# Performance work log

Measured on AMD Instinct MI355X. Metric: run time of the kernel, lower is better.

Reference implementation:

```python
import jax, jax.numpy as jnp
import numpy as np

T, B, IN, H = 256, 64, 512, 1024

def setup_inputs() -> dict:
    key = jax.random.key(0)
    ks = jax.random.split(key, 8)
    s_in = 1.0 / np.sqrt(IN)
    s_h = 1.0 / np.sqrt(H)
    return {
        "inp": jax.random.normal(ks[0], (T, B, IN), jnp.float32),
        "img": jax.random.normal(ks[1], (B, H), jnp.float32),
        "Wxh": jax.random.uniform(ks[2], (4 * H, IN), jnp.float32, -s_in, s_in),
        "bxh": jax.random.uniform(ks[3], (4 * H,), jnp.float32, -s_in, s_in),
        "Whh": jax.random.uniform(ks[4], (4 * H, H), jnp.float32, -s_h, s_h),
        "bhh": jax.random.uniform(ks[5], (4 * H,), jnp.float32, -s_h, s_h),
        "Wout": jax.random.uniform(ks[6], (IN, H), jnp.float32, -s_h, s_h),
        "bout": jax.random.uniform(ks[7], (IN,), jnp.float32, -s_h, s_h),
    }

def reference(inp, img, Wxh, bxh, Whh, bhh, Wout, bout):
    t_len, b, _ = inp.shape
    h_dim = Whh.shape[1]
    img4 = jnp.concatenate([img, img, img, img], axis=1)  # [B, 4H]
    # precompute input projection for all timesteps: [T, B, 4H]
    xproj = jnp.einsum('tbi,gi->tbg', inp, Wxh) + bxh
    xproj = xproj.at[0].add(img4)

    def step(carry, xg):
        h, c = carry
        gates = xg + h @ Whh.T + bhh  # [B, 4H]
        i_g, f_g, g_g, o_g = jnp.split(gates, 4, axis=1)
        c = jax.nn.sigmoid(f_g) * c + jax.nn.sigmoid(i_g) * jnp.tanh(g_g)
        h = jax.nn.sigmoid(o_g) * jnp.tanh(c)
        return (h, c), h

    zeros = jnp.zeros((b, h_dim), inp.dtype)
    _, hs = jax.lax.scan(step, (zeros, zeros), xproj)  # hs: [T, B, H]
    out = jnp.einsum('tbh,vh->tbv', hs, Wout) + bout  # [T, B, IN]
    return jax.nn.log_softmax(out, axis=-1)
```

## Files before the change

### kernel.cpp

```cpp
#include <hip/hip_runtime.h>
#include <math.h>

#define T_LEN 256
#define B_SZ  64
#define IN_D  512
#define H_D   1024
#define G4    4096

typedef float  f32x4 __attribute__((ext_vector_type(4)));
typedef short  s16x8 __attribute__((ext_vector_type(8)));
typedef unsigned int u32x4 __attribute__((ext_vector_type(4)));
typedef unsigned short u16;
typedef unsigned int   u32;

__device__ __forceinline__ void gl_lds16(const void* g, void* l) {
  __builtin_amdgcn_global_load_lds(
      (const __attribute__((address_space(1))) unsigned int*)g,
      (__attribute__((address_space(3))) unsigned int*)l, 16, 0, 0);
}

__device__ __forceinline__ u16 f2bf(float f) {
  union { float f; unsigned u; } v; v.f = f;
  unsigned x = v.u;
  unsigned r = (x + 0x7fffu + ((x >> 16) & 1u)) >> 16;
  return (u16)r;
}
__device__ __forceinline__ float bf2f(u16 b) {
  union { unsigned u; float f; } v; v.u = ((unsigned)b) << 16;
  return v.f;
}
__device__ __forceinline__ float sigm(float x) {
  return 1.0f / (1.0f + __expf(-x));
}
__device__ __forceinline__ float tanh_f(float x) {
  float e = __expf(2.0f * x);
  return 1.0f - 2.0f / (e + 1.0f);
}

__global__ void cvt_f32_bf16(const float* __restrict__ src, u16* __restrict__ dst, int n) {
  int i = blockIdx.x * blockDim.x + threadIdx.x;
  int stride = gridDim.x * blockDim.x;
  for (; i < n; i += stride) dst[i] = f2bf(src[i]);
}

template<int KD, int EPI>
__launch_bounds__(256)
__global__ void gemm_bt(const u16* __restrict__ A, const u16* __restrict__ Bm,
                        const float* __restrict__ bias, const float* __restrict__ img,
                        u16* __restrict__ Cb, float* __restrict__ Cf, int Ncols) {
  __shared__ u16 sA[128 * 64];
  __shared__ u16 sB[128 * 64];
  const int tid  = threadIdx.x;
  const int wave = tid >> 6, lane = tid & 63;
  const int wm = wave >> 1, wn = wave & 1;
  const int mBase = blockIdx.y * 128;
  const int nBase = blockIdx.x * 128;

  f32x4 acc[4][4] = {};

  for (int k0 = 0; k0 < KD; k0 += 64) {
#pragma unroll
    for (int it = 0; it < 4; ++it) {
      int s = it * 256 + tid;
      int row = s >> 3, c = s & 7;
      int gc = c ^ (row & 7);
      const u16* ga = A  + (size_t)(mBase + row) * KD + k0 + gc * 8;
      const u16* gb = Bm + (size_t)(nBase + row) * KD + k0 + gc * 8;
      gl_lds16(ga, &sA[(it * 256 + wave * 64) * 8]);
      gl_lds16(gb, &sB[(it * 256 + wave * 64) * 8]);
    }
    __syncthreads();

    const int q = lane >> 4, rl = lane & 15;
#pragma unroll
    for (int ks = 0; ks < 64; ks += 32) {
      s16x8 af[4], bfr[4];
      int gcb = (ks >> 3) + q;
#pragma unroll
      for (int i = 0; i < 4; ++i) {
        int rowA = wm * 64 + i * 16 + rl;
        af[i]  = *(const s16x8*)&sA[rowA * 64 + (gcb ^ (rowA & 7)) * 8];
        int rowB = wn * 64 + i * 16 + rl;
        bfr[i] = *(const s16x8*)&sB[rowB * 64 + (gcb ^ (rowB & 7)) * 8];
      }
#pragma unroll
      for (int i = 0; i < 4; ++i)
#pragma unroll
        for (int j = 0; j < 4; ++j)
          acc[i][j] = __builtin_amdgcn_mfma_f32_16x16x32_bf16(af[i], bfr[j], acc[i][j], 0, 0, 0);
    }
    __syncthreads();
  }

#pragma unroll
  for (int i = 0; i < 4; ++i) {
    int rbase = mBase + wm * 64 + i * 16 + ((lane >> 4) << 2);
#pragma unroll
    for (int j = 0; j < 4; ++j) {
      int col = nBase + wn * 64 + j * 16 + (lane & 15);
      float bc = bias[col];
#pragma unroll
      for (int r = 0; r < 4; ++r) {
        int row = rbase + r;
        float v = acc[i][j][r] + bc;
        if (EPI == 0) {
          if (row < B_SZ) v += img[row * H_D + (col & (H_D - 1))];
          Cb[(size_t)row * Ncols + col] = f2bf(v);
        } else {
          Cf[(size_t)row * Ncols + col] = v;
        }
      }
    }
  }
}

__launch_bounds__(256, 1)
__global__ void lstm_rec(const u16* __restrict__ WhhB, const u16* __restrict__ xproj,
                         const float* __restrict__ bhh, u32* __restrict__ hs32,
                         int* __restrict__ flags) {
  __shared__ u16  sH[16 * 1024];
  __shared__ float sGp[16][16][17];

  const int tid  = threadIdx.x;
  const int wave = tid >> 6, lane = tid & 63;
  const int grp = blockIdx.x >> 6;
  const int wg  = blockIdx.x & 63;
  const int bBase = grp * 16;
  const int colBase = wg * 16;
  const int q = lane >> 4, rl = lane & 15;

  s16x8 wf[4][8];
  {
    const u16* wb = WhhB + (size_t)(colBase + rl) * H_D + wave * 256 + q * 8;
#pragma unroll
    for (int g = 0; g < 4; ++g)
#pragma unroll
      for (int m = 0; m < 8; ++m)
        wf[g][m] = *(const s16x8*)(wb + (size_t)g * H_D * H_D + m * 32);
  }

  float cst = 0.f;
  const int ub = tid >> 4, uc = tid & 15;
  const int gb = bBase + ub;
  const int gcol = colBase + uc;
  const float bh_i = bhh[0 * H_D + gcol], bh_f = bhh[1 * H_D + gcol];
  const float bh_g = bhh[2 * H_D + gcol], bh_o = bhh[3 * H_D + gcol];

  for (int t = 0; t < T_LEN; ++t) {
    const u16* xp = xproj + ((size_t)t * B_SZ + gb) * G4;
    float gi_ = bf2f(xp[0 * H_D + gcol]) + bh_i;
    float gf_ = bf2f(xp[1 * H_D + gcol]) + bh_f;
    float gg_ = bf2f(xp[2 * H_D + gcol]) + bh_g;
    float go_ = bf2f(xp[3 * H_D + gcol]) + bh_o;

    if (t > 0) {
      if (tid < 64) {
        const int* fp = flags + (t - 1) * 256 + grp * 64 + tid;
        while (__hip_atomic_load(fp, __ATOMIC_RELAXED, __HIP_MEMORY_SCOPE_AGENT) == 0)
          __builtin_amdgcn_s_sleep(1);
      }
      __syncthreads();

      u32x4 v[8];
      const u32* hp = hs32 + (size_t)(t - 1) * B_SZ * 512 + (size_t)bBase * 512;
#pragma unroll
      for (int j = 0; j < 8; ++j) {
        int cid = j * 256 + tid;
        const u32* p = hp + (cid >> 7) * 512 + (cid & 127) * 4;
        asm volatile("global_load_dwordx4 %0, %1, off sc1"
                     : "=v"(v[j]) : "v"(p) : "memory");
      }
      asm volatile("s_waitcnt vmcnt(0)" ::: "memory");
#pragma unroll
      for (int j = 0; j < 8; ++j) {
        int cid = j * 256 + tid;
        int r = cid >> 7, c = cid & 127;
        *(s16x8*)&sH[r * 1024 + (c ^ (r & 7)) * 8] = *(s16x8*)&v[j];
      }
      __syncthreads();

      f32x4 a0 = {}, a1 = {}, a2 = {}, a3 = {};
#pragma unroll
      for (int m = 0; m < 8; ++m) {
        int chunk = wave * 32 + m * 4 + q;
        s16x8 afr = *(const s16x8*)&sH[rl * 1024 + ((chunk ^ (rl & 7))) * 8];
        a0 = __builtin_amdgcn_mfma_f32_16x16x32_bf16(afr, wf[0][m], a0, 0, 0, 0);
        a1 = __builtin_amdgcn_mfma_f32_16x16x32_bf16(afr, wf[1][m], a1, 0, 0, 0);
        a2 = __builtin_amdgcn_mfma_f32_16x16x32_bf16(afr, wf[2][m], a2, 0, 0, 0);
        a3 = __builtin_amdgcn_mfma_f32_16x16x32_bf16(afr, wf[3][m], a3, 0, 0, 0);
      }
#pragma unroll
      for (int r = 0; r < 4; ++r) {
        int row = (lane >> 4) * 4 + r;
        sGp[wave * 4 + 0][row][lane & 15] = a0[r];
        sGp[wave * 4 + 1][row][lane & 15] = a1[r];
        sGp[wave * 4 + 2][row][lane & 15] = a2[r];
        sGp[wave * 4 + 3][row][lane & 15] = a3[r];
      }
      __syncthreads();
      gi_ += sGp[0][ub][uc] + sGp[4][ub][uc] + sGp[8][ub][uc]  + sGp[12][ub][uc];
      gf_ += sGp[1][ub][uc] + sGp[5][ub][uc] + sGp[9][ub][uc]  + sGp[13][ub][uc];
      gg_ += sGp[2][ub][uc] + sGp[6][ub][uc] + sGp[10][ub][uc] + sGp[14][ub][uc];
      go_ += sGp[3][ub][uc] + sGp[7][ub][uc] + sGp[11][ub][uc] + sGp[15][ub][uc];
    }

    cst = sigm(gf_) * cst + sigm(gi_) * tanh_f(gg_);
    float h = sigm(go_) * tanh_f(cst);

    u32 b = f2bf(h);
    u32 p1 = (u32)__shfl_xor((int)b, 1);
    u32 w0 = b | (p1 << 16);
    u32 w1 = (u32)__shfl_xor((int)w0, 2);
    u32 w2 = (u32)__shfl_xor((int)w0, 4);
    u32 w3 = (u32)__shfl_xor((int)w1, 4);
    if ((tid & 7) == 0) {
      u32x4 pk = {w0, w1, w2, w3};
      u32* dst = hs32 + ((size_t)t * B_SZ + gb) * 512 + (gcol >> 1);
      asm volatile("global_store_dwordx4 %0, %1, off sc1"
                   :: "v"(dst), "v"(pk) : "memory");
    }
    __builtin_amdgcn_s_waitcnt(0);
    __syncthreads();
    if (tid == 0)
      __hip_atomic_store(&flags[t * 256 + grp * 64 + wg], 1,
                         __ATOMIC_RELAXED, __HIP_MEMORY_SCOPE_AGENT);
  }
}

__launch_bounds__(256)
__global__ void logsoftmax_rows(float* __restrict__ out) {
  __shared__ float red[8];
  float* p = out + (size_t)blockIdx.x * IN_D;
  const int tid = threadIdx.x;
  float v0 = p[tid], v1 = p[tid + 256];
  float m = fmaxf(v0, v1);
#pragma unroll
  for (int off = 32; off > 0; off >>= 1) m = fmaxf(m, __shfl_down(m, off));
  if ((tid & 63) == 0) red[tid >> 6] = m;
  __syncthreads();
  m = fmaxf(fmaxf(red[0], red[1]), fmaxf(red[2], red[3]));
  float e = __expf(v0 - m) + __expf(v1 - m);
#pragma unroll
  for (int off = 32; off > 0; off >>= 1) e += __shfl_down(e, off);
  if ((tid & 63) == 0) red[4 + (tid >> 6)] = e;
  __syncthreads();
  float ls = m + logf(red[4] + red[5] + red[6] + red[7]);
  p[tid] = v0 - ls;
  p[tid + 256] = v1 - ls;
}

extern "C" void kernel_launch(void* const* d_in, const int* in_sizes, int n_in,
                              void* d_out, int out_size, void* d_ws, size_t ws_size,
                              hipStream_t stream) {
  const float* inp  = (const float*)d_in[0];
  const float* img  = (const float*)d_in[1];
  const float* Wxh  = (const float*)d_in[2];
  const float* bxh  = (const float*)d_in[3];
  const float* Whh  = (const float*)d_in[4];
  const float* bhh  = (const float*)d_in[5];
  const float* Wout = (const float*)d_in[6];
  const float* bout = (const float*)d_in[7];
  float* out = (float*)d_out;

  char* ws = (char*)d_ws;
  u16* inpB   = (u16*)(ws);
  u16* WxhB   = (u16*)(ws + 16777216);
  u16* WhhB   = (u16*)(ws + 20971520);
  u16* WoutB  = (u16*)(ws + 29360128);
  u16* xprojB = (u16*)(ws + 30408704);
  u16* hsB    = (u16*)(ws + 164626432);
  int* flags  = (int*)(ws + 198180864);

  cvt_f32_bf16<<<2048, 256, 0, stream>>>(inp,  inpB,  T_LEN * B_SZ * IN_D);
  cvt_f32_bf16<<<2048, 256, 0, stream>>>(Wxh,  WxhB,  G4 * IN_D);
  cvt_f32_bf16<<<2048, 256, 0, stream>>>(Whh,  WhhB,  G4 * H_D);
  cvt_f32_bf16<<<2048, 256, 0, stream>>>(Wout, WoutB, IN_D * H_D);
  hipMemsetAsync(flags, 0, T_LEN * 256 * sizeof(int), stream);

  gemm_bt<IN_D, 0><<<dim3(G4 / 128, 16384 / 128), 256, 0, stream>>>(
      inpB, WxhB, bxh, img, xprojB, nullptr, G4);

  lstm_rec<<<256, 256, 0, stream>>>(WhhB, xprojB, bhh, (u32*)hsB, flags);

  gemm_bt<H_D, 1><<<dim3(IN_D / 128, 16384 / 128), 256, 0, stream>>>(
      hsB, WoutB, bout, nullptr, nullptr, out, IN_D);

  logsoftmax_rows<<<16384, 256, 0, stream>>>(out);
}
```

Measured before the change: 1.077 ms.

## Replace flag-based step sync with sentinel-polled hidden-state data

Drops the per-block flag arrays, their spin waits, the end-of-step barrier and the atomic stores. Instead the hidden-state buffer is pre-filled with an all-ones sentinel, and each block re-reads any 16-byte chunk of the previous step's h until no sentinel remains. This removes a round trip of flag publish and poll plus two barriers per timestep on the serial critical path. The cost is an extra fill kernel over the hs buffer. Correctness relies on 16-byte stores being seen atomically and on 0xFFFF never appearing as a real bf16 value; that value is a NaN encoding, which a tanh-bounded h should not produce.

```diff
diff --git a/kernel.cpp b/kernel.cpp
--- a/kernel.cpp
+++ b/kernel.cpp
@@ -41,6 +41,16 @@
   int i = blockIdx.x * blockDim.x + threadIdx.x;
   int stride = gridDim.x * blockDim.x;
   for (; i < n; i += stride) dst[i] = f2bf(src[i]);
+}
+
+__global__ void fill_sentinel(u32* __restrict__ p, int n4) {
+  int i = blockIdx.x * blockDim.x + threadIdx.x;
+  int stride = gridDim.x * blockDim.x;
+  u32x4 s = {0xFFFFFFFFu, 0xFFFFFFFFu, 0xFFFFFFFFu, 0xFFFFFFFFu};
+  for (; i < n4; i += stride) {
+    u32* dst = p + (size_t)i * 4;
+    asm volatile("global_store_dwordx4 %0, %1, off sc1" :: "v"(dst), "v"(s) : "memory");
+  }
 }
 
 template<int KD, int EPI>
@@ -116,8 +126,7 @@
 
 __launch_bounds__(256, 1)
 __global__ void lstm_rec(const u16* __restrict__ WhhB, const u16* __restrict__ xproj,
-                         const float* __restrict__ bhh, u32* __restrict__ hs32,
-                         int* __restrict__ flags) {
+                         const float* __restrict__ bhh, u32* __restrict__ hs32) {
   __shared__ u16  sH[16 * 1024];
   __shared__ float sGp[16][16][17];
 
@@ -154,13 +163,6 @@
     float go_ = bf2f(xp[3 * H_D + gcol]) + bh_o;
 
     if (t > 0) {
-      if (tid < 64) {
-        const int* fp = flags + (t - 1) * 256 + grp * 64 + tid;
-        while (__hip_atomic_load(fp, __ATOMIC_RELAXED, __HIP_MEMORY_SCOPE_AGENT) == 0)
-          __builtin_amdgcn_s_sleep(1);
-      }
-      __syncthreads();
-
       u32x4 v[8];
       const u32* hp = hs32 + (size_t)(t - 1) * B_SZ * 512 + (size_t)bBase * 512;
 #pragma unroll
@@ -171,6 +173,26 @@
                      : "=v"(v[j]) : "v"(p) : "memory");
       }
       asm volatile("s_waitcnt vmcnt(0)" ::: "memory");
+      for (;;) {
+        u32 bad = 0;
+#pragma unroll
+        for (int j = 0; j < 8; ++j) {
+          bool st = (v[j][0] == 0xFFFFFFFFu) | (v[j][1] == 0xFFFFFFFFu) |
+                    (v[j][2] == 0xFFFFFFFFu) | (v[j][3] == 0xFFFFFFFFu);
+          bad |= st ? (1u << j) : 0u;
+        }
+        if (!bad) break;
+#pragma unroll
+        for (int j = 0; j < 8; ++j) {
+          if (bad & (1u << j)) {
+            int cid = j * 256 + tid;
+            const u32* p = hp + (cid >> 7) * 512 + (cid & 127) * 4;
+            asm volatile("global_load_dwordx4 %0, %1, off sc1"
+                         : "=v"(v[j]) : "v"(p) : "memory");
+          }
+        }
+        asm volatile("s_waitcnt vmcnt(0)" ::: "memory");
+      }
 #pragma unroll
       for (int j = 0; j < 8; ++j) {
         int cid = j * 256 + tid;
@@ -219,12 +241,8 @@
       asm volatile("global_store_dwordx4 %0, %1, off sc1"
                    :: "v"(dst), "v"(pk) : "memory");
     }
-    __builtin_amdgcn_s_waitcnt(0);
-    __syncthreads();
-    if (tid == 0)
-      __hip_atomic_store(&flags[t * 256 + grp * 64 + wg], 1,
-                         __ATOMIC_RELAXED, __HIP_MEMORY_SCOPE_AGENT);
-  }
+  }
+  asm volatile("s_waitcnt vmcnt(0)" ::: "memory");
 }
 
 __launch_bounds__(256)
@@ -269,18 +287,18 @@
   u16* WoutB  = (u16*)(ws + 29360128);
   u16* xprojB = (u16*)(ws + 30408704);
   u16* hsB    = (u16*)(ws + 164626432);
-  int* flags  = (int*)(ws + 198180864);
+
+  fill_sentinel<<<2048, 256, 0, stream>>>((u32*)hsB, T_LEN * B_SZ * 512 / 4);
 
   cvt_f32_bf16<<<2048, 256, 0, stream>>>(inp,  inpB,  T_LEN * B_SZ * IN_D);
   cvt_f32_bf16<<<2048, 256, 0, stream>>>(Wxh,  WxhB,  G4 * IN_D);
   cvt_f32_bf16<<<2048, 256, 0, stream>>>(Whh,  WhhB,  G4 * H_D);
   cvt_f32_bf16<<<2048, 256, 0, stream>>>(Wout, WoutB, IN_D * H_D);
-  hipMemsetAsync(flags, 0, T_LEN * 256 * sizeof(int), stream);
 
   gemm_bt<IN_D, 0><<<dim3(G4 / 128, 16384 / 128), 256, 0, stream>>>(
       inpB, WxhB, bxh, img, xprojB, nullptr, G4);
 
-  lstm_rec<<<256, 256, 0, stream>>>(WhhB, xprojB, bhh, (u32*)hsB, flags);
+  lstm_rec<<<256, 256, 0, stream>>>(WhhB, xprojB, bhh, (u32*)hsB);
 
   gemm_bt<H_D, 1><<<dim3(IN_D / 128, 16384 / 128), 256, 0, stream>>>(
       hsB, WoutB, bout, nullptr, nullptr, out, IN_D);
```

Result: faster. 1.022 ms (-5.1%).
